# Kernel optimization log

Measured on AMD Instinct MI355X. Metric: run time of the kernel, lower is better.

Reference implementation:

```python
import jax, jax.numpy as jnp
import numpy as np

D_MODEL = 1024
NHEAD = 16
HEAD_DIM = D_MODEL // NHEAD


def setup_inputs() -> dict:
    key = jax.random.key(0)
    ks = jax.random.split(key, 7)
    N, S, E = 2, 2048, D_MODEL
    query = jax.random.normal(ks[0], (N, S, E), dtype=jnp.float32)
    key_t = jax.random.normal(ks[1], (N, S, E), dtype=jnp.float32)
    value = jax.random.normal(ks[2], (N, S, E), dtype=jnp.float32)
    # nn.Linear default init scale ~ 1/sqrt(fan_in)
    s = 1.0 / np.sqrt(E)
    w_in = jax.random.uniform(ks[3], (3 * E, E), jnp.float32, -s, s)
    b_in = jax.random.uniform(ks[4], (3 * E,), jnp.float32, -s, s)
    w_o = jax.random.uniform(ks[5], (E, E), jnp.float32, -s, s)
    b_o = jax.random.uniform(ks[6], (E,), jnp.float32, -s, s)
    return {"query": query, "key": key_t, "value": value,
            "w_in": w_in, "b_in": b_in, "w_o": w_o, "b_o": b_o}


def reference(query, key, value, w_in, b_in, w_o, b_o):
    # NOTE: the torch module computes q,k,v all from `query` (self-attention);
    # the `key`/`value` args are ignored by its forward math.
    N, S, E = query.shape
    H, Dh = NHEAD, HEAD_DIM
    qkv = query @ w_in.T + b_in                      # (N, S, 3E)
    q, k, v = jnp.split(qkv, 3, axis=-1)
    def heads(x):
        return x.reshape(N, S, H, Dh).transpose(0, 2, 1, 3)  # (N, H, S, Dh)
    q, k, v = heads(q), heads(k), heads(v)
    scale = 1.0 / jnp.sqrt(jnp.asarray(Dh, query.dtype))
    scores = jnp.einsum('bhqd,bhkd->bhqk', q, k) * scale     # (N, H, S, S)
    attn = jax.nn.softmax(scores, axis=-1)
    out = jnp.einsum('bhqk,bhkd->bhqd', attn, v)             # (N, H, S, Dh)
    out = out.transpose(0, 2, 1, 3).reshape(N, S, E)
    return out @ w_o.T + b_o
```

## Files before the change

### kernel.cpp

```cpp
#include <hip/hip_runtime.h>
#include <hip/hip_bf16.h>
#include <stdint.h>

#define NB   2
#define SEQ  2048
#define EMB  1024
#define NH   16
#define DH   64
#define MR   (NB*SEQ)
#define E3   (3*EMB)
#define CSC  (0.125f * 1.44269504f)

typedef __attribute__((ext_vector_type(8))) short bf16x8;
typedef __attribute__((ext_vector_type(4))) float f32x4;
typedef __attribute__((ext_vector_type(16))) float f32x16;

__device__ __forceinline__ unsigned short f2bf(float f) {
  unsigned u = __float_as_uint(f);
  unsigned r = (u + 0x7FFF + ((u >> 16) & 1)) >> 16;
  return (unsigned short)r;
}
__device__ __forceinline__ unsigned pack2(float lo, float hi) {
  return (unsigned)f2bf(lo) | ((unsigned)f2bf(hi) << 16);
}
__device__ __forceinline__ float bf2f(unsigned short s) {
  return __uint_as_float(((unsigned)s) << 16);
}
__device__ __forceinline__ unsigned cvtpk(float lo, float hi) {
  unsigned r;
  asm("v_cvt_pk_bf16_f32 %0, %1, %2" : "=v"(r) : "v"(lo), "v"(hi));
  return r;
}

__device__ __forceinline__ void gld16(const unsigned short* g, unsigned short* l) {
  __builtin_amdgcn_global_load_lds(
      (const __attribute__((address_space(1))) unsigned int*)g,
      (__attribute__((address_space(3))) unsigned int*)l,
      16, 0, 0);
}

__device__ __forceinline__ void lgkm0_bar() {
  asm volatile("s_waitcnt lgkmcnt(0)" ::: "memory");
  __builtin_amdgcn_s_barrier();
}
__device__ __forceinline__ void wait_vm4() {
  asm volatile("s_waitcnt vmcnt(4)" ::: "memory");
  __builtin_amdgcn_sched_barrier(0);
}
__device__ __forceinline__ void wait_vm0() {
  asm volatile("s_waitcnt vmcnt(0)" ::: "memory");
  __builtin_amdgcn_sched_barrier(0);
}

__global__ void cvt_all(const float* __restrict__ q,
                        const float* __restrict__ w_in,
                        const float* __restrict__ w_o,
                        unsigned short* __restrict__ Xbf,
                        unsigned short* __restrict__ Winbf,
                        unsigned short* __restrict__ Wobf) {
  int b = blockIdx.x;
  const float* src; unsigned short* dst; int off;
  if (b < 2048)      { src = q;    dst = Xbf;   off = b; }
  else if (b < 3584) { src = w_in; dst = Winbf; off = b - 2048; }
  else               { src = w_o;  dst = Wobf;  off = b - 3584; }
  int i = (off * 256 + threadIdx.x) * 8;
  float4 a = *(const float4*)(src + i);
  float4 c = *(const float4*)(src + i + 4);
  uint4 o;
  o.x = pack2(a.x, a.y);
  o.y = pack2(a.z, a.w);
  o.z = pack2(c.x, c.y);
  o.w = pack2(c.z, c.w);
  *(uint4*)(dst + i) = o;
}

template<int BN, bool OUT_F32>
__global__ __launch_bounds__(256) void gemm_bt(
    const unsigned short* __restrict__ A,
    const unsigned short* __restrict__ Bt,
    const float* __restrict__ bias,
    void* __restrict__ Cout,
    int K, int ldc, int scale_cols) {
  constexpr int NR = BN / 32;
  constexpr int WNT = BN / 2;
  __shared__ unsigned short As[4096];
  __shared__ unsigned short Bs[BN * 32];
  const int tid  = threadIdx.x;
  const int lane = tid & 63;
  const int w    = tid >> 6;
  const int wm = w >> 1, wn = w & 1;
  const int g = lane >> 4, li = lane & 15;
  const int rowBase = blockIdx.x * 128;
  const int colBase = blockIdx.y * BN;

  f32x4 acc[4][NR];
#pragma unroll
  for (int m = 0; m < 4; ++m)
#pragma unroll
    for (int nn = 0; nn < NR; ++nn) { acc[m][nn][0]=0.f; acc[m][nn][1]=0.f; acc[m][nn][2]=0.f; acc[m][nn][3]=0.f; }

  const unsigned short* Ag = A  + (size_t)(rowBase + (tid >> 2)) * K + (tid & 3) * 8;
  const unsigned short* Bg = Bt + (size_t)(colBase + (tid >> 2)) * K + (tid & 3) * 8;

  for (int k0 = 0; k0 < K; k0 += 32) {
    __syncthreads();
    gld16(Ag + k0,                As + tid * 8);
    gld16(Ag + (size_t)64*K + k0, As + 2048 + tid * 8);
    gld16(Bg + k0,                Bs + tid * 8);
    if (BN == 128)
      gld16(Bg + (size_t)64*K + k0, Bs + 2048 + tid * 8);
    __syncthreads();

    bf16x8 af[4], bfv[NR];
#pragma unroll
    for (int m = 0; m < 4; ++m)
      af[m] = *(const bf16x8*)&As[(wm*64 + m*16 + li) * 32 + g * 8];
#pragma unroll
    for (int nn = 0; nn < NR; ++nn)
      bfv[nn] = *(const bf16x8*)&Bs[(wn*WNT + nn*16 + li) * 32 + g * 8];
#pragma unroll
    for (int m = 0; m < 4; ++m)
#pragma unroll
      for (int nn = 0; nn < NR; ++nn)
        acc[m][nn] = __builtin_amdgcn_mfma_f32_16x16x32_bf16(af[m], bfv[nn], acc[m][nn], 0, 0, 0);
  }

#pragma unroll
  for (int nn = 0; nn < NR; ++nn) {
    const int col = colBase + wn*WNT + nn*16 + li;
    const float bv = bias[col];
    const float sc = (col < scale_cols) ? CSC : 1.0f;
#pragma unroll
    for (int m = 0; m < 4; ++m) {
      const int r0 = rowBase + wm*64 + m*16 + g*4;
#pragma unroll
      for (int r = 0; r < 4; ++r) {
        float v = (acc[m][nn][r] + bv) * sc;
        if (OUT_F32) ((float*)Cout)[(size_t)(r0 + r) * ldc + col] = v;
        else ((unsigned short*)Cout)[(size_t)(r0 + r) * ldc + col] = f2bf(v);
      }
    }
  }
}

__global__ __launch_bounds__(256, 2) void attn32(
    const unsigned short* __restrict__ qkv,
    unsigned short* __restrict__ x2) {
  __shared__ unsigned short smem[24576];
  char* LB = (char*)smem;

  const int tid  = threadIdx.x;
  const int lane = tid & 63;
  const int w    = tid >> 6;
  const int hi   = lane >> 5;
  const int l31  = lane & 31;
  const int slot = blockIdx.x;
  const int bid  = (slot & 7) * 64 + (slot >> 3);
  const int qb = bid & 15, h = (bid >> 4) & 15, n = bid >> 8;
  const size_t rowN = (size_t)n * SEQ;
  const int vp_ = tid & 31, dblk = tid >> 5;
  const int vps = (vp_ & ~6) | ((vp_ & 2) << 1) | ((vp_ & 4) >> 1);

  bf16x8 qf[4];
  {
    const size_t qr = rowN + qb*128 + w*32 + l31;
#pragma unroll
    for (int kc = 0; kc < 4; ++kc)
      qf[kc] = *(const bf16x8*)&qkv[qr * E3 + h*64 + kc*16 + hi*8];
  }

  f32x16 ZEROV;
#pragma unroll
  for (int i = 0; i < 16; ++i) ZEROV[i] = 0.f;
  f32x16 acc0 = ZEROV, acc1 = ZEROV;
  float ssum[8];
#pragma unroll
  for (int i = 0; i < 8; ++i) ssum[i] = 0.f;

  uint4 pv0, pv1;
  auto stageK = [&](int kt, int buf) {
#pragma unroll
    for (int p = 0; p < 2; ++p) {
      int r = p*32 + (tid >> 3);
      int ch = (tid & 7) ^ (r & 7);
      gld16(&qkv[(rowN + kt + r) * E3 + EMB + h*64 + ch*8],
            &smem[buf*4096 + p*2048 + tid*8]);
    }
  };
  auto loadV = [&](int kt) {
    const unsigned short* vp = &qkv[(rowN + kt + 2*vp_) * E3 + 2*EMB + h*64 + dblk*8];
    pv0 = *(const uint4*)vp;
    pv1 = *(const uint4*)(vp + E3);
  };
  auto writeV = [&](int vb) {
    const unsigned short* s0 = (const unsigned short*)&pv0;
    const unsigned short* s1 = (const unsigned short*)&pv1;
#pragma unroll
    for (int j = 0; j < 8; ++j) {
      int d = dblk*8 + j;
      unsigned val = (unsigned)s0[j] | ((unsigned)s1[j] << 16);
      *(unsigned*)(LB + 16384 + vb*8192 + d*128 + (((vps>>2) ^ (d&7)) << 4) + (vps&3)*4) = val;
    }
  };
  auto QK = [&](int cur, f32x16& o0, f32x16& o1) {
    const char* Kb = LB + cur*8192;
    bf16x8 ka[4], kb[4];
#pragma unroll
    for (int kc = 0; kc < 4; ++kc) {
      const int sw = ((kc*2 + hi) ^ (l31 & 7)) << 4;
      ka[kc] = *(const bf16x8*)(Kb + l31*128 + sw);
      kb[kc] = *(const bf16x8*)(Kb + 4096 + l31*128 + sw);
    }
    __builtin_amdgcn_s_setprio(1);
    o0 = __builtin_amdgcn_mfma_f32_32x32x16_bf16(ka[0], qf[0], ZEROV, 0, 0, 0);
    o1 = __builtin_amdgcn_mfma_f32_32x32x16_bf16(kb[0], qf[0], ZEROV, 0, 0, 0);
#pragma unroll
    for (int kc = 1; kc < 4; ++kc) {
      o0 = __builtin_amdgcn_mfma_f32_32x32x16_bf16(ka[kc], qf[kc], o0, 0, 0, 0);
      o1 = __builtin_amdgcn_mfma_f32_32x32x16_bf16(kb[kc], qf[kc], o1, 0, 0, 0);
    }
    __builtin_amdgcn_s_setprio(0);
  };
  auto SMPV = [&](int vb, f32x16& z0, f32x16& z1) {
#pragma unroll
    for (int i = 0; i < 16; ++i) {
      z0[i] = __builtin_amdgcn_exp2f(z0[i]);
      z1[i] = __builtin_amdgcn_exp2f(z1[i]);
    }
#pragma unroll
    for (int i = 0; i < 8; ++i)
      ssum[i] += (z0[2*i] + z0[2*i+1]) + (z1[2*i] + z1[2*i+1]);
    bf16x8 pf[4];
    {
      union { bf16x8 v; unsigned u[4]; } r0_, r1_, r2_, r3_;
#pragma unroll
      for (int j = 0; j < 4; ++j) {
        r0_.u[j] = cvtpk(z0[2*j],     z0[2*j + 1]);
        r1_.u[j] = cvtpk(z0[8 + 2*j], z0[9 + 2*j]);
        r2_.u[j] = cvtpk(z1[2*j],     z1[2*j + 1]);
        r3_.u[j] = cvtpk(z1[8 + 2*j], z1[9 + 2*j]);
      }
      pf[0] = r0_.v; pf[1] = r1_.v; pf[2] = r2_.v; pf[3] = r3_.v;
    }
    const char* Vb = LB + 16384 + vb*8192;
    __builtin_amdgcn_s_setprio(1);
#pragma unroll
    for (int c = 0; c < 4; ++c) {
      const int sw = ((c*2 + hi) ^ (l31 & 7)) << 4;
      bf16x8 va = *(const bf16x8*)(Vb + l31*128 + sw);
      bf16x8 vb_ = *(const bf16x8*)(Vb + 4096 + l31*128 + sw);
      acc0 = __builtin_amdgcn_mfma_f32_32x32x16_bf16(va,  pf[c], acc0, 0, 0, 0);
      acc1 = __builtin_amdgcn_mfma_f32_32x32x16_bf16(vb_, pf[c], acc1, 0, 0, 0);
    }
    __builtin_amdgcn_s_setprio(0);
  };

  f32x16 zA0, zA1, zB0, zB1;

  loadV(0); stageK(0, 0); writeV(0);
  lgkm0_bar();
  loadV(64); stageK(64, 1);
  wait_vm4();
  QK(0, zA0, zA1);
  writeV(1);
  lgkm0_bar();

  for (int t = 1; t < 31; t += 2) {
    loadV((t + 1) * 64); stageK((t + 1) * 64, (t + 1) & 1);
    wait_vm4();
    QK(t & 1, zB0, zB1);
    SMPV((t - 1) & 3, zA0, zA1);
    writeV((t + 1) & 3);
    lgkm0_bar();
    loadV((t + 2) * 64); stageK((t + 2) * 64, (t + 2) & 1);
    wait_vm4();
    QK((t + 1) & 1, zA0, zA1);
    SMPV(t & 3, zB0, zB1);
    writeV((t + 2) & 3);
    lgkm0_bar();
  }

  wait_vm0();
  QK(1, zB0, zB1);
  SMPV(30 & 3, zA0, zA1);
  SMPV(31 & 3, zB0, zB1);

#pragma unroll
  for (int st = 4; st; st >>= 1)
#pragma unroll
    for (int i = 0; i < st; ++i) ssum[i] += ssum[i + st];
  float lsum = ssum[0] + __shfl_xor(ssum[0], 32);

  __syncthreads();
  float rn = 1.0f / lsum;
  const int qrow_l = w*32 + l31;
#pragma unroll
  for (int dt = 0; dt < 2; ++dt) {
#pragma unroll
    for (int r = 0; r < 16; r += 2) {
      float v0 = (dt ? acc1[r]   : acc0[r])   * rn;
      float v1 = (dt ? acc1[r+1] : acc0[r+1]) * rn;
      int d = dt*32 + (r & 3) + 8*(r >> 2) + 4*hi;
      unsigned val = pack2(v0, v1);
      int col32 = d >> 1;
      int g = col32 >> 2;
      *(unsigned*)(LB + qrow_l*128 + ((g ^ (qrow_l & 7)) << 4) + (col32 & 3)*4) = val;
    }
  }
  __syncthreads();
  {
    int row = tid >> 1;
    size_t orow = (rowN + qb*128 + row) * EMB + h*64;
#pragma unroll
    for (int i = 0; i < 4; ++i) {
      int gg = (tid & 1)*4 + i;
      uint4 v = *(const uint4*)(LB + row*128 + ((gg ^ (row & 7)) << 4));
      *(uint4*)&x2[orow + gg*8] = v;
    }
  }
}

extern "C" void kernel_launch(void* const* d_in, const int* in_sizes, int n_in,
                              void* d_out, int out_size, void* d_ws, size_t ws_size,
                              hipStream_t stream) {
  const float* q    = (const float*)d_in[0];
  const float* w_in = (const float*)d_in[3];
  const float* b_in = (const float*)d_in[4];
  const float* w_o  = (const float*)d_in[5];
  const float* b_o  = (const float*)d_in[6];

  char* ws = (char*)d_ws;
  unsigned short* Wobf  = (unsigned short*)(ws);
  unsigned short* Xbf   = (unsigned short*)(ws + 2097152);
  unsigned short* Winbf = (unsigned short*)(ws + 10485760);
  unsigned short* QKV   = (unsigned short*)(ws + 16777216);
  unsigned short* X2    = (unsigned short*)(ws + 41943040);

  cvt_all<<<4096, 256, 0, stream>>>(q, w_in, w_o, Xbf, Winbf, Wobf);

  gemm_bt<128, false><<<dim3(32, 24), 256, 0, stream>>>(Xbf, Winbf, b_in, (void*)QKV, EMB, E3, 1024);
  attn32<<<NB * NH * (SEQ / 128), 256, 0, stream>>>(QKV, X2);
  gemm_bt<64, true><<<dim3(32, 16), 256, 0, stream>>>(X2, Wobf, b_o, d_out, EMB, EMB, 0);
}
```

Baseline: 116.1 us.

## Replace QKV projection GEMM with 256x256-tile 8-wave pipelined kernel

Adds a new QKV projection GEMM that uses 256x256 output tiles, 512 threads (8 waves) and 128KB of LDS split into double buffers. Global-to-LDS loads for the next K-slices are interleaved with MFMA phases, and it uses barriers, s_setprio and partial vmcnt waits to overlap memory with compute. The aim is more data reuse per tile and better latency hiding than the previous 128x128 gemm_bt. In exchange it runs at one block per CU with only 192 blocks, and it relies on fragile hand-scheduled wait counts.

New measurement: 116.1 us. No clear change (+0.0%).

```diff
diff --git a/kernel.cpp b/kernel.cpp
--- a/kernel.cpp
+++ b/kernel.cpp
@@ -74,6 +74,130 @@
   *(uint4*)(dst + i) = o;
 }
 
+#define G8_PHASE(BUFA, BUFB, MH, NHH, STB, STSRC, STROW, STKT, STX, STISB, WAITE) \
+  {                                                                            \
+    bf16x8 af[4][2], bfr[2][2];                                                \
+    _Pragma("unroll")                                                          \
+    for (int mf = 0; mf < 4; ++mf)                                             \
+      _Pragma("unroll")                                                        \
+      for (int ks = 0; ks < 2; ++ks) {                                         \
+        int rt = wm*128 + (MH)*64 + mf*16 + li;                                \
+        int c  = ks*4 + g;                                                     \
+        af[mf][ks] = *(const bf16x8*)&smem[(BUFA) + rt*64 + ((c ^ (rt&7))<<3)];\
+      }                                                                        \
+    _Pragma("unroll")                                                          \
+    for (int nf = 0; nf < 2; ++nf)                                             \
+      _Pragma("unroll")                                                        \
+      for (int ks = 0; ks < 2; ++ks) {                                         \
+        int ct = wn*64 + (NHH)*32 + nf*16 + li;                                \
+        int c  = ks*4 + g;                                                     \
+        bfr[nf][ks] = *(const bf16x8*)&smem[(BUFB) + ct*64 + ((c ^ (ct&7))<<3)];\
+      }                                                                        \
+    _Pragma("unroll")                                                          \
+    for (int j = 0; j < 2; ++j) {                                              \
+      int rt = (STISB) ? (j*128 + ((sr>>5)<<6) + (STX)*32 + (sr&31))           \
+                       : (j*128 + (STX)*64 + sr);                              \
+      gld16((STSRC) + (size_t)((STROW) + rt)*1024 + (STKT) + sch*8,            \
+            &smem[(STB) + rt*64 + sc8*8]);                                     \
+    }                                                                          \
+    asm volatile("" ::: "memory");                                             \
+    __builtin_amdgcn_s_barrier();                                              \
+    __builtin_amdgcn_s_setprio(1);                                             \
+    _Pragma("unroll")                                                          \
+    for (int mf = 0; mf < 4; ++mf)                                             \
+      _Pragma("unroll")                                                        \
+      for (int nf = 0; nf < 2; ++nf)                                           \
+        _Pragma("unroll")                                                      \
+        for (int ks = 0; ks < 2; ++ks)                                         \
+          acc[(MH)*4+mf][(NHH)*2+nf] = __builtin_amdgcn_mfma_f32_16x16x32_bf16(\
+              af[mf][ks], bfr[nf][ks], acc[(MH)*4+mf][(NHH)*2+nf], 0, 0, 0);   \
+    __builtin_amdgcn_s_setprio(0);                                             \
+    if (WAITE) asm volatile("s_waitcnt vmcnt(6)" ::: "memory");                \
+    asm volatile("" ::: "memory");                                             \
+    __builtin_amdgcn_s_barrier();                                              \
+  }
+
+__global__ __launch_bounds__(512, 1) void gemm8p(
+    const unsigned short* __restrict__ A,
+    const unsigned short* __restrict__ Bt,
+    const float* __restrict__ bias,
+    unsigned short* __restrict__ C) {
+  __shared__ unsigned short smem[65536];
+  const int tid = threadIdx.x;
+  const int lane = tid & 63;
+  const int w = tid >> 6;
+  const int wm = w >> 2, wn = w & 3;
+  const int g = lane >> 4, li = lane & 15;
+  const int bid = blockIdx.x;
+  const int rowBase = (bid & 15) * 256;
+  const int colBase = (bid >> 4) * 256;
+  const int sr  = tid >> 3;
+  const int sc8 = tid & 7;
+  const int sch = sc8 ^ (sr & 7);
+
+  const int A0 = 0, B0 = 16384, A1 = 32768, B1 = 49152;
+
+  f32x4 acc[8][4];
+#pragma unroll
+  for (int am = 0; am < 8; ++am)
+#pragma unroll
+    for (int an = 0; an < 4; ++an) { acc[am][an][0]=0.f; acc[am][an][1]=0.f; acc[am][an][2]=0.f; acc[am][an][3]=0.f; }
+
+  auto stageA = [&](int base, int trow, int kt, int X) {
+#pragma unroll
+    for (int j = 0; j < 2; ++j) {
+      int rt = j*128 + X*64 + sr;
+      gld16(A + (size_t)(trow + rt)*1024 + kt + sch*8, &smem[base + rt*64 + sc8*8]);
+    }
+  };
+  auto stageB = [&](int base, int trow, int kt, int X) {
+#pragma unroll
+    for (int j = 0; j < 2; ++j) {
+      int rt = j*128 + ((sr>>5)<<6) + X*32 + (sr&31);
+      gld16(Bt + (size_t)(trow + rt)*1024 + kt + sch*8, &smem[base + rt*64 + sc8*8]);
+    }
+  };
+
+  stageA(A0, rowBase, 0, 0);
+  stageB(B0, colBase, 0, 0);
+  stageA(A0, rowBase, 0, 1);
+  stageB(B0, colBase, 0, 1);
+  stageB(B1, colBase, 64, 0);
+  stageA(A1, rowBase, 64, 0);
+  asm volatile("s_waitcnt vmcnt(0)" ::: "memory");
+  __builtin_amdgcn_s_barrier();
+
+  for (int i = 0; i < 8; ++i) {
+    const int kt1 = (2*i + 1) * 64;
+    const int kt2 = (2*i + 2 > 15 ? 15 : 2*i + 2) * 64;
+    const int kt3 = (2*i + 3 > 15 ? 15 : 2*i + 3) * 64;
+    G8_PHASE(A0, B0, 0, 0, A1, A,  rowBase, kt1, 1, 0, true)
+    G8_PHASE(A0, B0, 1, 0, B1, Bt, colBase, kt1, 1, 1, false)
+    G8_PHASE(A0, B0, 0, 1, B0, Bt, colBase, kt2, 0, 1, true)
+    G8_PHASE(A0, B0, 1, 1, A0, A,  rowBase, kt2, 0, 0, false)
+    G8_PHASE(A1, B1, 0, 0, A0, A,  rowBase, kt2, 1, 0, true)
+    G8_PHASE(A1, B1, 1, 0, B0, Bt, colBase, kt2, 1, 1, false)
+    G8_PHASE(A1, B1, 0, 1, B1, Bt, colBase, kt3, 0, 1, true)
+    G8_PHASE(A1, B1, 1, 1, A1, A,  rowBase, kt3, 0, 0, false)
+  }
+
+  asm volatile("s_waitcnt vmcnt(0)" ::: "memory");
+
+#pragma unroll
+  for (int an = 0; an < 4; ++an) {
+    const int col = colBase + wn*64 + (an>>1)*32 + (an&1)*16 + li;
+    const float bv = bias[col];
+    const float sc = (col < 1024) ? CSC : 1.0f;
+#pragma unroll
+    for (int am = 0; am < 8; ++am) {
+      const int r0 = rowBase + wm*128 + (am>>2)*64 + (am&3)*16 + g*4;
+#pragma unroll
+      for (int rr = 0; rr < 4; ++rr)
+        C[(size_t)(r0 + rr) * E3 + col] = f2bf((acc[am][an][rr] + bv) * sc);
+    }
+  }
+}
+
 template<int BN, bool OUT_F32>
 __global__ __launch_bounds__(256) void gemm_bt(
     const unsigned short* __restrict__ A,
@@ -338,7 +462,7 @@
 
   cvt_all<<<4096, 256, 0, stream>>>(q, w_in, w_o, Xbf, Winbf, Wobf);
 
-  gemm_bt<128, false><<<dim3(32, 24), 256, 0, stream>>>(Xbf, Winbf, b_in, (void*)QKV, EMB, E3, 1024);
+  gemm8p<<<192, 512, 0, stream>>>(Xbf, Winbf, b_in, QKV);
   attn32<<<NB * NH * (SEQ / 128), 256, 0, stream>>>(QKV, X2);
   gemm_bt<64, true><<<dim3(32, 16), 256, 0, stream>>>(X2, Wobf, b_o, d_out, EMB, EMB, 0);
 }
```
